# Performance work log

Measured on AMD Instinct MI355X. Metric: run time of the kernel, lower is better.

The kernel has to match this reference:

```python
import jax, jax.numpy as jnp
import numpy as np

BLK = 128          # stk blocking
HID = 1024         # hidden_size
FFN = 4096         # ffn_hidden_size per expert
NE = 8             # moe_num_experts
TOK = 8192         # padded tokens (multiple of BLK)


def setup_inputs() -> dict:
    key = jax.random.key(0)
    k1, k2, k3 = jax.random.split(key, 3)
    x = jax.random.normal(k1, (TOK, HID), dtype=jnp.float32)
    w1 = jax.random.normal(k2, (NE * FFN, HID), dtype=jnp.float32) * 0.02
    n_row_blocks = TOK // BLK          # 64
    cols_per_expert = FFN // BLK       # 32
    # dMoE topology: each token row-block is assigned one expert; its nonzero
    # column blocks are all ffn blocks of that expert.
    expert_assign = jax.random.randint(k3, (n_row_blocks,), 0, NE)
    row_indices = jnp.repeat(jnp.arange(n_row_blocks), cols_per_expert)
    column_indices = (expert_assign[:, None] * cols_per_expert
                      + jnp.arange(cols_per_expert)[None, :]).reshape(-1)
    return {
        "x": x,
        "w1": w1,
        "row_indices": row_indices.astype(jnp.int32),     # [nnz]
        "column_indices": column_indices.astype(jnp.int32),  # [nnz]
        "block": BLK,
    }


def reference(x, w1, row_indices, column_indices, block):
    # sdd(x, w1.T, topo): out block k = x_block[row_indices[k]] @ w1_block[column_indices[k]].T
    hid = x.shape[1]
    xb = x.reshape(-1, block, hid)    # [n_row_blocks, blk, hid]
    wb = w1.reshape(-1, block, hid)   # [n_col_blocks, blk, hid]
    # [nnz, blk, blk] block-sparse data of the output matrix
    return jnp.einsum('kbh,kch->kbc', xb[row_indices], wb[column_indices])
```

## Files before the change

### kernel.cpp

```cpp
#include <hip/hip_runtime.h>
#include <hip/hip_bf16.h>
#include <stdint.h>

#define HID 1024
#define BLKDIM 128
#define BKT 32
#define NKT (HID / BKT)
#define NBUF 3

using short8 = __attribute__((ext_vector_type(8))) short;
using f32x4  = __attribute__((ext_vector_type(4))) float;
using f32x4v = __attribute__((ext_vector_type(4))) float;

__device__ __forceinline__ uint32_t bfround(float f) {
    uint32_t u = __builtin_bit_cast(uint32_t, f);
    return (u + 0x7FFFu + ((u >> 16) & 1u)) >> 16;
}

__device__ __forceinline__ void gld16(const ushort* g, const ushort* lds_base) {
    __builtin_amdgcn_global_load_lds(
        (const __attribute__((address_space(1))) void*)g,
        (__attribute__((address_space(3))) void*)lds_base, 16, 0, 0);
}

__global__ __launch_bounds__(256)
void cvt_bf16_kernel(const float* __restrict__ src, uint4* __restrict__ dst, int n8) {
    int i = blockIdx.x * blockDim.x + threadIdx.x;
    if (i >= n8) return;
    const f32x4v* s = reinterpret_cast<const f32x4v*>(src) + (size_t)i * 2;
    f32x4v v0 = __builtin_nontemporal_load(s);
    f32x4v v1 = __builtin_nontemporal_load(s + 1);
    uint4 w;
    w.x = bfround(v0.x) | (bfround(v0.y) << 16);
    w.y = bfround(v0.z) | (bfround(v0.w) << 16);
    w.z = bfround(v1.x) | (bfround(v1.y) << 16);
    w.w = bfround(v1.z) | (bfround(v1.w) << 16);
    dst[i] = w;
}

__global__ __launch_bounds__(512, 4)
void sdd_pipe2_kernel(const ushort* __restrict__ xb, const ushort* __restrict__ wb,
                      const int* __restrict__ rind, const int* __restrict__ cind,
                      float* __restrict__ out) {
    __shared__ ushort lds[NBUF * BLKDIM * BKT + NBUF * 2 * BLKDIM * BKT];

    int g = blockIdx.x;
    const int nwg = gridDim.x;
    if ((nwg & 7) == 0) {
        const int cpx = nwg >> 3;
        g = (g & 7) * cpx + (g >> 3);
    }
    const int k0 = g * 2;
    const int r  = rind[k0];

    const int t = threadIdx.x;
    const int w = t >> 6;
    const int l = t & 63;

    ushort* sAb = lds;
    ushort* sBb = lds + NBUF * BLKDIM * BKT;

    const int unx   = (l & 7) ^ ((l >> 3) & 7);
    const int rin16 = 2 * (l >> 3) + (unx >> 2);
    const int kofs  = (unx & 3) * 8;

    const ushort* agb = xb + (size_t)(r * BLKDIM + w * 16 + rin16) * HID + kofs;
    const int cblk = cind[k0 + (w >> 2)];
    const ushort* bgb = wb + (size_t)(cblk * BLKDIM + (w & 3) * 32 + rin16) * HID + kofs;

    const int wr   = (w >> 2) * 64;
    const int wcol = (w & 3) * 64;
    const int ps_l = (((l >> 4) + ((l & 1) << 2)) ^ ((l & 15) >> 1)) * 8;
    const int rhalf = (l & 15) >> 1;

    int aoff[4], boff[4];
#pragma unroll
    for (int m = 0; m < 4; ++m) aoff[m] = (wr / 2 + m * 8 + rhalf) * 64 + ps_l;
#pragma unroll
    for (int n = 0; n < 4; ++n) boff[n] = (wcol / 2 + n * 8 + rhalf) * 64 + ps_l;

    f32x4 acc[4][4];
#pragma unroll
    for (int m = 0; m < 4; ++m)
#pragma unroll
        for (int n = 0; n < 4; ++n)
            acc[m][n] = (f32x4){0.f, 0.f, 0.f, 0.f};

    auto stage = [&](int b, int kt) {
        gld16(agb + kt * BKT, &sAb[b * 4096 + w * 512]);
        gld16(bgb + kt * BKT,                      &sBb[b * 8192 + (2 * w) * 512]);
        gld16(bgb + (size_t)16 * HID + kt * BKT,   &sBb[b * 8192 + (2 * w + 1) * 512]);
    };

    stage(0, 0);
    stage(1, 1);
    asm volatile("s_waitcnt vmcnt(3)" ::: "memory");
    __builtin_amdgcn_s_barrier();
    __builtin_amdgcn_sched_barrier(0);

    for (int kt = 0; kt < NKT; ++kt) {
        const int cur = kt % 3;
        const int nxt = (kt + 2) % 3;
        const bool pre = (kt + 2) < NKT;
        const ushort* sa = &sAb[cur * 4096];
        const ushort* sb = &sBb[cur * 8192];

        short8 aF[4], bF[4];
#pragma unroll
        for (int m = 0; m < 4; ++m)
            aF[m] = *reinterpret_cast<const short8*>(&sa[aoff[m]]);
#pragma unroll
        for (int n = 0; n < 4; ++n)
            bF[n] = *reinterpret_cast<const short8*>(&sb[boff[n]]);
        if (pre) stage(nxt, kt + 2);
        __builtin_amdgcn_s_setprio(1);
#pragma unroll
        for (int m = 0; m < 4; ++m)
#pragma unroll
            for (int n = 0; n < 4; ++n)
                acc[m][n] = __builtin_amdgcn_mfma_f32_16x16x32_bf16(aF[m], bF[n], acc[m][n], 0, 0, 0);
        __builtin_amdgcn_s_setprio(0);

        if (pre) asm volatile("s_waitcnt vmcnt(3)" ::: "memory");
        else     asm volatile("s_waitcnt vmcnt(0)" ::: "memory");
        __builtin_amdgcn_s_barrier();
        __builtin_amdgcn_sched_barrier(0);
    }

    const int blk = (w & 3) >> 1;
    float* op = out + (size_t)(k0 + blk) * (BLKDIM * BLKDIM);
    const int colbase = (wcol & 64) ? 64 : 0;
    float* scr = reinterpret_cast<float*>(lds) + w * 1152;

#pragma unroll
    for (int m = 0; m < 4; ++m) {
#pragma unroll
        for (int n = 0; n < 4; ++n)
#pragma unroll
            for (int j = 0; j < 4; ++j)
                scr[((l >> 4) * 4 + j) * 72 + n * 16 + (l & 15)] = acc[m][n][j];
#pragma unroll
        for (int rg = 0; rg < 4; ++rg) {
            const int tr = rg * 4 + (l >> 4);
            f32x4 v = *reinterpret_cast<const f32x4*>(&scr[tr * 72 + (l & 15) * 4]);
            __builtin_nontemporal_store(v,
                reinterpret_cast<f32x4*>(&op[(size_t)(wr + m * 16 + tr) * BLKDIM
                                             + colbase + (l & 15) * 4]));
        }
    }
}

__device__ __forceinline__ void store16f(ushort* dst, float4 v0, float4 v1, float4 v2, float4 v3) {
    uint4 w0, w1;
    w0.x = bfround(v0.x) | (bfround(v0.y) << 16);
    w0.y = bfround(v0.z) | (bfround(v0.w) << 16);
    w0.z = bfround(v1.x) | (bfround(v1.y) << 16);
    w0.w = bfround(v1.z) | (bfround(v1.w) << 16);
    w1.x = bfround(v2.x) | (bfround(v2.y) << 16);
    w1.y = bfround(v2.z) | (bfround(v2.w) << 16);
    w1.z = bfround(v3.x) | (bfround(v3.y) << 16);
    w1.w = bfround(v3.z) | (bfround(v3.w) << 16);
    uint4* d = reinterpret_cast<uint4*>(dst);
    d[0] = w0; d[1] = w1;
}

__global__ __launch_bounds__(256, 2)
void sdd_bf16_kernel(const float* __restrict__ x, const float* __restrict__ w1,
                     const int* __restrict__ rind, const int* __restrict__ cind,
                     float* __restrict__ out) {
    __shared__ ushort sA[2][BLKDIM * 32];
    __shared__ ushort sB[2][BLKDIM * 32];
    const int k = blockIdx.x;
    const int t = threadIdx.x;
    const int r = rind[k];
    const int c = cind[k];
    const float* Abase = x  + (size_t)r * BLKDIM * HID;
    const float* Bbase = w1 + (size_t)c * BLKDIM * HID;
    const int srow = t >> 1, shalf = t & 1;
    const float* aptr = Abase + (size_t)srow * HID + shalf * 16;
    const float* bptr = Bbase + (size_t)srow * HID + shalf * 16;
    const int soff = srow * 32 + shalf * 16;
    const int wv = t >> 6, lane = t & 63;
    const int wr = (wv >> 1) * 64, wc = (wv & 1) * 64;
    const int lr = lane & 15, lk = (lane >> 4) * 8;
    f32x4 acc[4][4];
#pragma unroll
    for (int m = 0; m < 4; ++m)
#pragma unroll
        for (int n = 0; n < 4; ++n) acc[m][n] = (f32x4){0.f, 0.f, 0.f, 0.f};
    float4 ra[4], rb[4];
#pragma unroll
    for (int i = 0; i < 4; ++i) {
        ra[i] = *reinterpret_cast<const float4*>(aptr + i * 4);
        rb[i] = *reinterpret_cast<const float4*>(bptr + i * 4);
    }
    store16f(&sA[0][soff], ra[0], ra[1], ra[2], ra[3]);
    store16f(&sB[0][soff], rb[0], rb[1], rb[2], rb[3]);
    __syncthreads();
    for (int kt = 0; kt < 32; ++kt) {
        const int cur = kt & 1;
        if (kt + 1 < 32) {
            const float* ap = aptr + (kt + 1) * 32;
            const float* bp = bptr + (kt + 1) * 32;
#pragma unroll
            for (int i = 0; i < 4; ++i) {
                ra[i] = *reinterpret_cast<const float4*>(ap + i * 4);
                rb[i] = *reinterpret_cast<const float4*>(bp + i * 4);
            }
        }
        const ushort* sa = sA[cur];
        const ushort* sb = sB[cur];
        short8 aF[4], bF[4];
#pragma unroll
        for (int m = 0; m < 4; ++m) aF[m] = *reinterpret_cast<const short8*>(&sa[(wr + m * 16 + lr) * 32 + lk]);
#pragma unroll
        for (int n = 0; n < 4; ++n) bF[n] = *reinterpret_cast<const short8*>(&sb[(wc + n * 16 + lr) * 32 + lk]);
#pragma unroll
        for (int m = 0; m < 4; ++m)
#pragma unroll
            for (int n = 0; n < 4; ++n)
                acc[m][n] = __builtin_amdgcn_mfma_f32_16x16x32_bf16(aF[m], bF[n], acc[m][n], 0, 0, 0);
        if (kt + 1 < 32) {
            store16f(&sA[cur ^ 1][soff], ra[0], ra[1], ra[2], ra[3]);
            store16f(&sB[cur ^ 1][soff], rb[0], rb[1], rb[2], rb[3]);
        }
        __syncthreads();
    }
    float* op = out + (size_t)k * (BLKDIM * BLKDIM);
    const int rbase = wr + (lane >> 4) * 4;
#pragma unroll
    for (int m = 0; m < 4; ++m)
#pragma unroll
        for (int n = 0; n < 4; ++n) {
            const int col = wc + n * 16 + lr;
#pragma unroll
            for (int j = 0; j < 4; ++j)
                op[(size_t)(rbase + m * 16 + j) * BLKDIM + col] = acc[m][n][j];
        }
}

extern "C" void kernel_launch(void* const* d_in, const int* in_sizes, int n_in,
                              void* d_out, int out_size, void* d_ws, size_t ws_size,
                              hipStream_t stream) {
    const float* x  = (const float*)d_in[0];
    const float* w1 = (const float*)d_in[1];
    const int* ri   = (const int*)d_in[2];
    const int* ci   = (const int*)d_in[3];
    float* out      = (float*)d_out;
    const int nnz   = in_sizes[2];
    const int nx    = in_sizes[0];
    const int nw    = in_sizes[1];

    const size_t need = ((size_t)nx + (size_t)nw) * sizeof(ushort);
    if (ws_size >= need && (nnz & 1) == 0) {
        ushort* xb = (ushort*)d_ws;
        ushort* wb = xb + nx;
        const int nx8 = nx / 8, nw8 = nw / 8;
        hipLaunchKernelGGL(cvt_bf16_kernel, dim3((nx8 + 255) / 256), dim3(256), 0, stream,
                           x, (uint4*)xb, nx8);
        hipLaunchKernelGGL(cvt_bf16_kernel, dim3((nw8 + 255) / 256), dim3(256), 0, stream,
                           w1, (uint4*)wb, nw8);
        hipLaunchKernelGGL(sdd_pipe2_kernel, dim3(nnz / 2), dim3(512), 0, stream,
                           xb, wb, ri, ci, out);
    } else {
        hipLaunchKernelGGL(sdd_bf16_kernel, dim3(nnz), dim3(256), 0, stream,
                           x, w1, ri, ci, out);
    }
}
```

Baseline: 141.2 us.

## Replace LDS-staged GEMM with direct global-to-register MFMA operand loads

The 512-thread kernel that covered two output blocks through a triple-buffered LDS pipeline is replaced by a 256-thread kernel with one output block per workgroup. Each wave now loads its MFMA operands straight from global memory into registers, double-buffered across k-steps, and uses LDS only for the output transpose. This drops the LDS staging and the per-iteration barriers. In exchange, the A and B tiles shared between waves are no longer reused on chip, so global and L2 traffic rise, and the per-lane 16-byte loads are strided and less coalesced.

```diff
diff --git a/kernel.cpp b/kernel.cpp
--- a/kernel.cpp
+++ b/kernel.cpp
@@ -4,9 +4,6 @@
 
 #define HID 1024
 #define BLKDIM 128
-#define BKT 32
-#define NKT (HID / BKT)
-#define NBUF 3
 
 using short8 = __attribute__((ext_vector_type(8))) short;
 using f32x4  = __attribute__((ext_vector_type(4))) float;
@@ -15,12 +12,6 @@
 __device__ __forceinline__ uint32_t bfround(float f) {
     uint32_t u = __builtin_bit_cast(uint32_t, f);
     return (u + 0x7FFFu + ((u >> 16) & 1u)) >> 16;
-}
-
-__device__ __forceinline__ void gld16(const ushort* g, const ushort* lds_base) {
-    __builtin_amdgcn_global_load_lds(
-        (const __attribute__((address_space(1))) void*)g,
-        (__attribute__((address_space(3))) void*)lds_base, 16, 0, 0);
 }
 
 __global__ __launch_bounds__(256)
@@ -38,11 +29,11 @@
     dst[i] = w;
 }
 
-__global__ __launch_bounds__(512, 4)
-void sdd_pipe2_kernel(const ushort* __restrict__ xb, const ushort* __restrict__ wb,
+__global__ __launch_bounds__(256, 2)
+void sdd_nolds_kernel(const ushort* __restrict__ xb, const ushort* __restrict__ wb,
                       const int* __restrict__ rind, const int* __restrict__ cind,
                       float* __restrict__ out) {
-    __shared__ ushort lds[NBUF * BLKDIM * BKT + NBUF * 2 * BLKDIM * BKT];
+    __shared__ float scr[4 * 1152];
 
     int g = blockIdx.x;
     const int nwg = gridDim.x;
@@ -50,34 +41,19 @@
         const int cpx = nwg >> 3;
         g = (g & 7) * cpx + (g >> 3);
     }
-    const int k0 = g * 2;
-    const int r  = rind[k0];
+    const int r = rind[g];
+    const int c = cind[g];
 
     const int t = threadIdx.x;
     const int w = t >> 6;
     const int l = t & 63;
-
-    ushort* sAb = lds;
-    ushort* sBb = lds + NBUF * BLKDIM * BKT;
-
-    const int unx   = (l & 7) ^ ((l >> 3) & 7);
-    const int rin16 = 2 * (l >> 3) + (unx >> 2);
-    const int kofs  = (unx & 3) * 8;
-
-    const ushort* agb = xb + (size_t)(r * BLKDIM + w * 16 + rin16) * HID + kofs;
-    const int cblk = cind[k0 + (w >> 2)];
-    const ushort* bgb = wb + (size_t)(cblk * BLKDIM + (w & 3) * 32 + rin16) * HID + kofs;
-
-    const int wr   = (w >> 2) * 64;
-    const int wcol = (w & 3) * 64;
-    const int ps_l = (((l >> 4) + ((l & 1) << 2)) ^ ((l & 15) >> 1)) * 8;
-    const int rhalf = (l & 15) >> 1;
-
-    int aoff[4], boff[4];
-#pragma unroll
-    for (int m = 0; m < 4; ++m) aoff[m] = (wr / 2 + m * 8 + rhalf) * 64 + ps_l;
-#pragma unroll
-    for (int n = 0; n < 4; ++n) boff[n] = (wcol / 2 + n * 8 + rhalf) * 64 + ps_l;
+    const int wr   = (w >> 1) * 64;
+    const int wcol = (w & 1) * 64;
+    const int lr   = l & 15;
+    const int ksl  = (l >> 4) * 8;
+
+    const ushort* ax = xb + (size_t)(r * BLKDIM + wr   + lr) * HID + ksl;
+    const ushort* bx = wb + (size_t)(c * BLKDIM + wcol + lr) * HID + ksl;
 
     f32x4 acc[4][4];
 #pragma unroll
@@ -86,66 +62,53 @@
         for (int n = 0; n < 4; ++n)
             acc[m][n] = (f32x4){0.f, 0.f, 0.f, 0.f};
 
-    auto stage = [&](int b, int kt) {
-        gld16(agb + kt * BKT, &sAb[b * 4096 + w * 512]);
-        gld16(bgb + kt * BKT,                      &sBb[b * 8192 + (2 * w) * 512]);
-        gld16(bgb + (size_t)16 * HID + kt * BKT,   &sBb[b * 8192 + (2 * w + 1) * 512]);
-    };
-
-    stage(0, 0);
-    stage(1, 1);
-    asm volatile("s_waitcnt vmcnt(3)" ::: "memory");
-    __builtin_amdgcn_s_barrier();
-    __builtin_amdgcn_sched_barrier(0);
-
-    for (int kt = 0; kt < NKT; ++kt) {
-        const int cur = kt % 3;
-        const int nxt = (kt + 2) % 3;
-        const bool pre = (kt + 2) < NKT;
-        const ushort* sa = &sAb[cur * 4096];
-        const ushort* sb = &sBb[cur * 8192];
-
-        short8 aF[4], bF[4];
+    short8 a0[4], b0[4], a1[4], b1[4];
+
+#define LD4(dst, base, kt)                                                         \
+    _Pragma("unroll")                                                              \
+    for (int i = 0; i < 4; ++i)                                                    \
+        dst[i] = *reinterpret_cast<const short8*>((base) + (size_t)i * 16 * HID + (kt) * 32);
+
+    LD4(a0, ax, 0)
+    LD4(b0, bx, 0)
+
+    for (int kt = 0; kt < 32; kt += 2) {
+        LD4(a1, ax, kt + 1)
+        LD4(b1, bx, kt + 1)
 #pragma unroll
         for (int m = 0; m < 4; ++m)
-            aF[m] = *reinterpret_cast<const short8*>(&sa[aoff[m]]);
+#pragma unroll
+            for (int n = 0; n < 4; ++n)
+                acc[m][n] = __builtin_amdgcn_mfma_f32_16x16x32_bf16(a0[m], b0[n], acc[m][n], 0, 0, 0);
+        if (kt + 2 < 32) {
+            LD4(a0, ax, kt + 2)
+            LD4(b0, bx, kt + 2)
+        }
+#pragma unroll
+        for (int m = 0; m < 4; ++m)
+#pragma unroll
+            for (int n = 0; n < 4; ++n)
+                acc[m][n] = __builtin_amdgcn_mfma_f32_16x16x32_bf16(a1[m], b1[n], acc[m][n], 0, 0, 0);
+    }
+#undef LD4
+
+    float* op = out + (size_t)g * (BLKDIM * BLKDIM);
+    float* s  = scr + w * 1152;
+
+#pragma unroll
+    for (int m = 0; m < 4; ++m) {
 #pragma unroll
         for (int n = 0; n < 4; ++n)
-            bF[n] = *reinterpret_cast<const short8*>(&sb[boff[n]]);
-        if (pre) stage(nxt, kt + 2);
-        __builtin_amdgcn_s_setprio(1);
-#pragma unroll
-        for (int m = 0; m < 4; ++m)
-#pragma unroll
-            for (int n = 0; n < 4; ++n)
-                acc[m][n] = __builtin_amdgcn_mfma_f32_16x16x32_bf16(aF[m], bF[n], acc[m][n], 0, 0, 0);
-        __builtin_amdgcn_s_setprio(0);
-
-        if (pre) asm volatile("s_waitcnt vmcnt(3)" ::: "memory");
-        else     asm volatile("s_waitcnt vmcnt(0)" ::: "memory");
-        __builtin_amdgcn_s_barrier();
-        __builtin_amdgcn_sched_barrier(0);
-    }
-
-    const int blk = (w & 3) >> 1;
-    float* op = out + (size_t)(k0 + blk) * (BLKDIM * BLKDIM);
-    const int colbase = (wcol & 64) ? 64 : 0;
-    float* scr = reinterpret_cast<float*>(lds) + w * 1152;
-
-#pragma unroll
-    for (int m = 0; m < 4; ++m) {
-#pragma unroll
-        for (int n = 0; n < 4; ++n)
 #pragma unroll
             for (int j = 0; j < 4; ++j)
-                scr[((l >> 4) * 4 + j) * 72 + n * 16 + (l & 15)] = acc[m][n][j];
+                s[((l >> 4) * 4 + j) * 72 + n * 16 + (l & 15)] = acc[m][n][j];
 #pragma unroll
         for (int rg = 0; rg < 4; ++rg) {
             const int tr = rg * 4 + (l >> 4);
-            f32x4 v = *reinterpret_cast<const f32x4*>(&scr[tr * 72 + (l & 15) * 4]);
+            f32x4 v = *reinterpret_cast<const f32x4*>(&s[tr * 72 + (l & 15) * 4]);
             __builtin_nontemporal_store(v,
                 reinterpret_cast<f32x4*>(&op[(size_t)(wr + m * 16 + tr) * BLKDIM
-                                             + colbase + (l & 15) * 4]));
+                                             + wcol + (l & 15) * 4]));
         }
     }
 }
@@ -252,7 +215,7 @@
     const int nw    = in_sizes[1];
 
     const size_t need = ((size_t)nx + (size_t)nw) * sizeof(ushort);
-    if (ws_size >= need && (nnz & 1) == 0) {
+    if (ws_size >= need) {
         ushort* xb = (ushort*)d_ws;
         ushort* wb = xb + nx;
         const int nx8 = nx / 8, nw8 = nw / 8;
@@ -260,7 +223,7 @@
                            x, (uint4*)xb, nx8);
         hipLaunchKernelGGL(cvt_bf16_kernel, dim3((nw8 + 255) / 256), dim3(256), 0, stream,
                            w1, (uint4*)wb, nw8);
-        hipLaunchKernelGGL(sdd_pipe2_kernel, dim3(nnz / 2), dim3(512), 0, stream,
+        hipLaunchKernelGGL(sdd_nolds_kernel, dim3(nnz), dim3(256), 0, stream,
                            xb, wb, ri, ci, out);
     } else {
         hipLaunchKernelGGL(sdd_bf16_kernel, dim3(nnz), dim3(256), 0, stream,
```

After: 279.1 us. +97.7%, slower.

## Reorder workgroups by expert so blocks sharing weights run together

Applied to the files above, without the earlier changes.

Adds a single-workgroup scheduling kernel that groups token row-blocks by their assigned expert and builds a permutation of workgroup indices. Concurrently running workgroups then share the same expert weight column blocks, and consecutive columns interleave across rows, which is meant to improve L2/MALL reuse of W1 and X tiles. The schedule hardcodes the topology (64 row blocks, 32 columns per expert, 8 experts) and only runs when nnz and x size match the test shape. It also adds an extra serial launch on one thread.

```diff
diff --git a/kernel.cpp b/kernel.cpp
--- a/kernel.cpp
+++ b/kernel.cpp
@@ -38,9 +38,34 @@
     dst[i] = w;
 }
 
+__global__ void build_sched_kernel(const int* __restrict__ cind, int* __restrict__ perm) {
+    __shared__ int srb[64];
+    __shared__ int goff[9];
+    const int t = threadIdx.x;
+    if (t == 0) {
+        int er[64], cnt[8], off[8];
+        for (int e = 0; e < 8; ++e) cnt[e] = 0;
+        for (int r = 0; r < 64; ++r) { er[r] = (cind[r * 32] >> 5) & 7; cnt[er[r]]++; }
+        goff[0] = 0;
+        for (int e = 0; e < 8; ++e) { goff[e + 1] = goff[e] + cnt[e]; off[e] = goff[e]; }
+        for (int r = 0; r < 64; ++r) srb[off[er[r]]++] = r;
+    }
+    __syncthreads();
+    for (int g = t; g < 1024; g += blockDim.x) {
+        int e = 0;
+        while (g >= goff[e + 1] * 16) ++e;
+        const int ne = goff[e + 1] - goff[e];
+        const int local = g - goff[e] * 16;
+        const int j = local / ne;
+        const int idx = local - j * ne;
+        perm[g] = srb[goff[e] + idx] * 16 + j;
+    }
+}
+
 __global__ __launch_bounds__(512, 4)
 void sdd_pipe2_kernel(const ushort* __restrict__ xb, const ushort* __restrict__ wb,
                       const int* __restrict__ rind, const int* __restrict__ cind,
+                      const int* __restrict__ perm,
                       float* __restrict__ out) {
     __shared__ ushort lds[NBUF * BLKDIM * BKT + NBUF * 2 * BLKDIM * BKT];
 
@@ -50,6 +75,7 @@
         const int cpx = nwg >> 3;
         g = (g & 7) * cpx + (g >> 3);
     }
+    g = perm[g];
     const int k0 = g * 2;
     const int r  = rind[k0];
 
@@ -251,17 +277,19 @@
     const int nx    = in_sizes[0];
     const int nw    = in_sizes[1];
 
-    const size_t need = ((size_t)nx + (size_t)nw) * sizeof(ushort);
-    if (ws_size >= need && (nnz & 1) == 0) {
+    const size_t need = ((size_t)nx + (size_t)nw) * sizeof(ushort) + 4096 * sizeof(int);
+    if (ws_size >= need && nnz == 2048 && nx == 8388608) {
         ushort* xb = (ushort*)d_ws;
         ushort* wb = xb + nx;
+        int* perm  = (int*)(wb + nw);
         const int nx8 = nx / 8, nw8 = nw / 8;
         hipLaunchKernelGGL(cvt_bf16_kernel, dim3((nx8 + 255) / 256), dim3(256), 0, stream,
                            x, (uint4*)xb, nx8);
         hipLaunchKernelGGL(cvt_bf16_kernel, dim3((nw8 + 255) / 256), dim3(256), 0, stream,
                            w1, (uint4*)wb, nw8);
+        hipLaunchKernelGGL(build_sched_kernel, dim3(1), dim3(256), 0, stream, ci, perm);
         hipLaunchKernelGGL(sdd_pipe2_kernel, dim3(nnz / 2), dim3(512), 0, stream,
-                           xb, wb, ri, ci, out);
+                           xb, wb, ri, ci, perm, out);
     } else {
         hipLaunchKernelGGL(sdd_bf16_kernel, dim3(nnz), dim3(256), 0, stream,
                            x, w1, ri, ci, out);
```

Measured after the change: 135.9 us. 3.7% less time.
